# Kernel optimization log

Hardware: AMD Instinct MI355X
Metric: run time of the kernel (lower is better)

Reference implementation:

```python
import jax, jax.numpy as jnp
import numpy as np

DT = 1.0  # module init dt

def setup_inputs() -> dict:
    key = jax.random.key(0)
    k1, k2 = jax.random.split(key)
    x = jax.random.normal(k1, (8, 4096, 512), dtype=jnp.float32)
    w = jax.random.normal(k2, (512,), dtype=jnp.float32)
    return {"x": x, "w": w}

def reference(x, w):
    # h_t = h_{t-1} + dt*(x_t - relu(w)*h_{t-1}) = a*h_{t-1} + dt*x_t,  a = 1 - dt*relu(w)
    a = (1.0 - DT * jax.nn.relu(w)).astype(x.dtype)  # [d]
    h0 = jnp.zeros((x.shape[0], x.shape[2]), dtype=x.dtype)  # [b, d]
    xt = jnp.swapaxes(x, 0, 1)  # [t, b, d]

    def step(h, x_t):
        h_next = a * h + DT * x_t
        return h_next, h_next

    _, hs = jax.lax.scan(step, h0, xt)  # [t, b, d]
    return jnp.swapaxes(hs, 0, 1)  # [b, t, d] (return_sequences=True)
```

## Files before the change

### kernel.cpp

```cpp
#include <hip/hip_runtime.h>


#define RB 8
#define RT 4096
#define RD 512
#define DG (RD / 4)
#define TG 8
#define NTL (DG / TG)
#define CL 32
#define NC (RT / CL)
#define TPB 1024
#define PF 4
#define HB 1e15f

typedef float f32x4 __attribute__((ext_vector_type(4)));

__device__ __forceinline__ float sclamp(float v) {
    return fminf(fmaxf(v, -HB), HB);
}
__device__ __forceinline__ f32x4 sclamp4(f32x4 v) {
    v.x = sclamp(v.x); v.y = sclamp(v.y);
    v.z = sclamp(v.z); v.w = sclamp(v.w);
    return v;
}
__device__ __forceinline__ f32x4 ld4(const float4* __restrict__ p) {
    return *(const f32x4* __restrict__)p;
}
__device__ __forceinline__ f32x4 shfl4(f32x4 v, int src) {
    f32x4 r;
    r.x = __shfl(v.x, src, 64);
    r.y = __shfl(v.y, src, 64);
    r.z = __shfl(v.z, src, 64);
    r.w = __shfl(v.w, src, 64);
    return r;
}
__device__ __forceinline__ f32x4 relu_decay(float4 wq) {
    f32x4 a;
    a.x = 1.0f - fmaxf(wq.x, 0.0f);
    a.y = 1.0f - fmaxf(wq.y, 0.0f);
    a.z = 1.0f - fmaxf(wq.z, 0.0f);
    a.w = 1.0f - fmaxf(wq.w, 0.0f);
    return a;
}

__global__ void __launch_bounds__(TPB, 4)
rnn_fused3(const float4* __restrict__ x4, const float4* __restrict__ w4,
           float4* __restrict__ out4) {
    const int tid = threadIdx.x;
    const int g   = tid & (TG - 1);
    const int c   = tid >> 3;

    const int bid  = blockIdx.x;
    const int b    = bid >> 4;
    const int tile = bid & (NTL - 1);

    const f32x4 A1 = relu_decay(w4[tile * TG + g]);

    __shared__ f32x4 Wagg[NC * 9];
    __shared__ f32x4 CI[NC * 9];
    __shared__ f32x4 WinAgg[2 * 9];

    const size_t base = ((size_t)b * RT + (size_t)c * CL) * DG
                      + (size_t)(tile * TG + g);
    const float4* __restrict__ xb = x4 + base;

    {
        f32x4 v[PF];
#pragma unroll
        for (int k = 0; k < PF; ++k) v[k] = ld4(xb + (size_t)k * DG);
        f32x4 h = {0.f, 0.f, 0.f, 0.f};
#pragma unroll
        for (int bb = 0; bb < CL; bb += PF) {
            f32x4 n[PF];
            if (bb + PF < CL) {
#pragma unroll
                for (int k = 0; k < PF; ++k)
                    n[k] = ld4(xb + (size_t)(bb + PF + k) * DG);
            }
#pragma unroll
            for (int k = 0; k < PF; ++k) h = sclamp4(A1 * h + v[k]);
            if (bb + PF < CL) {
#pragma unroll
                for (int k = 0; k < PF; ++k) v[k] = n[k];
            }
        }
        Wagg[c * 9 + g] = h;
    }
    __syncthreads();

    {
        const int w  = tid >> 6;
        const int l  = tid & 63;
        const int g2 = w & (TG - 1);
        const int q  = w >> 3;
        const int cc = q * 64 + l;

        f32x4 B = relu_decay(w4[tile * TG + g2]);
#pragma unroll
        for (int i = 0; i < 5; ++i) B = sclamp4(B * B);

        f32x4 S = Wagg[cc * 9 + g2];
        f32x4 M = B;
#pragma unroll
        for (int s = 1; s < 64; s <<= 1) {
            f32x4 t = shfl4(S, l >= s ? l - s : l);
            S = (l >= s) ? sclamp4(M * t + S) : S;
            M = sclamp4(M * M);
        }
        if (l == 63) WinAgg[q * 9 + g2] = S;
        __syncthreads();

        f32x4 WC = {0.f, 0.f, 0.f, 0.f};
        if (q == 1) WC = WinAgg[0 * 9 + g2];
        const int n = l + 1;
        f32x4 P = {1.f, 1.f, 1.f, 1.f};
        f32x4 mm = B;
#pragma unroll
        for (int k = 0; k < 7; ++k) {
            if ((n >> k) & 1) P = sclamp4(P * mm);
            mm = sclamp4(mm * mm);
        }
        f32x4 Sf = sclamp4(S + P * WC);
        if (cc < NC - 1) CI[(cc + 1) * 9 + g2] = Sf;
        if (cc == 0)     CI[0 * 9 + g2] = (f32x4){0.f, 0.f, 0.f, 0.f};
    }
    __syncthreads();

    {
        float4* __restrict__ ob = out4 + base;
        f32x4 h = CI[c * 9 + g];
        f32x4 v[PF];
#pragma unroll
        for (int k = 0; k < PF; ++k) v[k] = ld4(xb + (size_t)k * DG);
#pragma unroll
        for (int bb = 0; bb < CL; bb += PF) {
            f32x4 n[PF];
            if (bb + PF < CL) {
#pragma unroll
                for (int k = 0; k < PF; ++k)
                    n[k] = ld4(xb + (size_t)(bb + PF + k) * DG);
            }
#pragma unroll
            for (int k = 0; k < PF; ++k) {
                h = sclamp4(A1 * h + v[k]);
                __builtin_nontemporal_store(
                    h, (f32x4*)(ob + (size_t)(bb + k) * DG));
            }
            if (bb + PF < CL) {
#pragma unroll
                for (int k = 0; k < PF; ++k) v[k] = n[k];
            }
        }
    }
}

extern "C" void kernel_launch(void* const* d_in, const int* in_sizes, int n_in,
                              void* d_out, int out_size, void* d_ws, size_t ws_size,
                              hipStream_t stream) {
    const float4* x4 = (const float4*)d_in[0];
    const float4* w4 = (const float4*)d_in[1];
    float4* o4 = (float4*)d_out;
    rnn_fused3<<<dim3(RB * NTL), dim3(TPB), 0, stream>>>(x4, w4, o4);
}
```

Before: 138.9 us.

## Split time axis across two blocks, recomputing first-half carry redundantly

The grid doubles to 256 blocks by splitting the sequence into two halves. Each second-half block redundantly scans the first half to get its carry-in, then both halves run the chunked scan with the chunk length halved. This exposes more parallelism on a GPU with many CUs, where 128 blocks left units idle. The cost is extra reads of x and extra compute for second-half blocks, which makes the work per block uneven.

```diff
diff --git a/kernel.cpp b/kernel.cpp
--- a/kernel.cpp
+++ b/kernel.cpp
@@ -7,8 +7,9 @@
 #define DG (RD / 4)
 #define TG 8
 #define NTL (DG / TG)
-#define CL 32
-#define NC (RT / CL)
+#define HT (RT / 2)
+#define CL 16
+#define NC (HT / CL)
 #define TPB 1024
 #define PF 4
 #define HB 1e15f
@@ -43,64 +44,94 @@
     return a;
 }
 
+__device__ __forceinline__ f32x4 chunk_scan(const float4* __restrict__ xb,
+                                            f32x4 A1) {
+    f32x4 v[PF];
+#pragma unroll
+    for (int k = 0; k < PF; ++k) v[k] = ld4(xb + (size_t)k * DG);
+    f32x4 h = {0.f, 0.f, 0.f, 0.f};
+#pragma unroll
+    for (int bb = 0; bb < CL; bb += PF) {
+        f32x4 n[PF];
+        if (bb + PF < CL) {
+#pragma unroll
+            for (int k = 0; k < PF; ++k)
+                n[k] = ld4(xb + (size_t)(bb + PF + k) * DG);
+        }
+#pragma unroll
+        for (int k = 0; k < PF; ++k) h = sclamp4(A1 * h + v[k]);
+        if (bb + PF < CL) {
+#pragma unroll
+            for (int k = 0; k < PF; ++k) v[k] = n[k];
+        }
+    }
+    return h;
+}
+
 __global__ void __launch_bounds__(TPB, 4)
-rnn_fused3(const float4* __restrict__ x4, const float4* __restrict__ w4,
-           float4* __restrict__ out4) {
+rnn_half(const float4* __restrict__ x4, const float4* __restrict__ w4,
+         float4* __restrict__ out4) {
     const int tid = threadIdx.x;
     const int g   = tid & (TG - 1);
     const int c   = tid >> 3;
 
     const int bid  = blockIdx.x;
-    const int b    = bid >> 4;
-    const int tile = bid & (NTL - 1);
+    const int hh   = bid >> 7;
+    const int p    = bid & 127;
+    const int b    = p >> 4;
+    const int tile = p & (NTL - 1);
 
     const f32x4 A1 = relu_decay(w4[tile * TG + g]);
 
     __shared__ f32x4 Wagg[NC * 9];
     __shared__ f32x4 CI[NC * 9];
     __shared__ f32x4 WinAgg[2 * 9];
+    __shared__ f32x4 Hc[TG];
 
-    const size_t base = ((size_t)b * RT + (size_t)c * CL) * DG
-                      + (size_t)(tile * TG + g);
-    const float4* __restrict__ xb = x4 + base;
+    const size_t tilebase = (size_t)b * RT * DG + (size_t)(tile * TG + g);
+    const float4* __restrict__ xb_own =
+        x4 + tilebase + (size_t)(hh * HT + c * CL) * DG;
 
-    {
-        f32x4 v[PF];
+    const int w  = tid >> 6;
+    const int l  = tid & 63;
+    const int g2 = w & (TG - 1);
+    const int q  = w >> 3;
+    const int cc = q * 64 + l;
+
+    f32x4 Bg2 = relu_decay(w4[tile * TG + g2]);
 #pragma unroll
-        for (int k = 0; k < PF; ++k) v[k] = ld4(xb + (size_t)k * DG);
-        f32x4 h = {0.f, 0.f, 0.f, 0.f};
+    for (int i = 0; i < 4; ++i) Bg2 = sclamp4(Bg2 * Bg2);
+
+    if (hh == 1) {
+        const float4* __restrict__ xb_f =
+            x4 + tilebase + (size_t)(c * CL) * DG;
+        Wagg[c * 9 + g] = chunk_scan(xb_f, A1);
+        __syncthreads();
+        {
+            f32x4 S = Wagg[cc * 9 + g2];
+            f32x4 M = Bg2;
 #pragma unroll
-        for (int bb = 0; bb < CL; bb += PF) {
-            f32x4 n[PF];
-            if (bb + PF < CL) {
-#pragma unroll
-                for (int k = 0; k < PF; ++k)
-                    n[k] = ld4(xb + (size_t)(bb + PF + k) * DG);
+            for (int s = 1; s < 64; s <<= 1) {
+                f32x4 t = shfl4(S, l >= s ? l - s : l);
+                S = (l >= s) ? sclamp4(M * t + S) : S;
+                M = sclamp4(M * M);
             }
-#pragma unroll
-            for (int k = 0; k < PF; ++k) h = sclamp4(A1 * h + v[k]);
-            if (bb + PF < CL) {
-#pragma unroll
-                for (int k = 0; k < PF; ++k) v[k] = n[k];
-            }
+            if (l == 63) WinAgg[q * 9 + g2] = S;
+            __syncthreads();
+            if (q == 1 && l == 63)
+                Hc[g2] = sclamp4(M * WinAgg[0 * 9 + g2] + S);
         }
-        Wagg[c * 9 + g] = h;
     }
     __syncthreads();
 
+    Wagg[c * 9 + g] = chunk_scan(xb_own, A1);
+    __syncthreads();
+
     {
-        const int w  = tid >> 6;
-        const int l  = tid & 63;
-        const int g2 = w & (TG - 1);
-        const int q  = w >> 3;
-        const int cc = q * 64 + l;
-
-        f32x4 B = relu_decay(w4[tile * TG + g2]);
-#pragma unroll
-        for (int i = 0; i < 5; ++i) B = sclamp4(B * B);
-
+        const f32x4 C0 = (hh == 1) ? Hc[g2]
+                                   : (f32x4){0.f, 0.f, 0.f, 0.f};
         f32x4 S = Wagg[cc * 9 + g2];
-        f32x4 M = B;
+        f32x4 M = Bg2;
 #pragma unroll
         for (int s = 1; s < 64; s <<= 1) {
             f32x4 t = shfl4(S, l >= s ? l - s : l);
@@ -110,11 +141,11 @@
         if (l == 63) WinAgg[q * 9 + g2] = S;
         __syncthreads();
 
-        f32x4 WC = {0.f, 0.f, 0.f, 0.f};
-        if (q == 1) WC = WinAgg[0 * 9 + g2];
+        f32x4 WC = C0;
+        if (q == 1) WC = sclamp4(M * C0 + WinAgg[0 * 9 + g2]);
         const int n = l + 1;
         f32x4 P = {1.f, 1.f, 1.f, 1.f};
-        f32x4 mm = B;
+        f32x4 mm = Bg2;
 #pragma unroll
         for (int k = 0; k < 7; ++k) {
             if ((n >> k) & 1) P = sclamp4(P * mm);
@@ -122,23 +153,24 @@
         }
         f32x4 Sf = sclamp4(S + P * WC);
         if (cc < NC - 1) CI[(cc + 1) * 9 + g2] = Sf;
-        if (cc == 0)     CI[0 * 9 + g2] = (f32x4){0.f, 0.f, 0.f, 0.f};
+        if (cc == 0)     CI[0 * 9 + g2] = C0;
     }
     __syncthreads();
 
     {
-        float4* __restrict__ ob = out4 + base;
+        float4* __restrict__ ob =
+            out4 + tilebase + (size_t)(hh * HT + c * CL) * DG;
         f32x4 h = CI[c * 9 + g];
         f32x4 v[PF];
 #pragma unroll
-        for (int k = 0; k < PF; ++k) v[k] = ld4(xb + (size_t)k * DG);
+        for (int k = 0; k < PF; ++k) v[k] = ld4(xb_own + (size_t)k * DG);
 #pragma unroll
         for (int bb = 0; bb < CL; bb += PF) {
             f32x4 n[PF];
             if (bb + PF < CL) {
 #pragma unroll
                 for (int k = 0; k < PF; ++k)
-                    n[k] = ld4(xb + (size_t)(bb + PF + k) * DG);
+                    n[k] = ld4(xb_own + (size_t)(bb + PF + k) * DG);
             }
 #pragma unroll
             for (int k = 0; k < PF; ++k) {
@@ -160,5 +192,5 @@
     const float4* x4 = (const float4*)d_in[0];
     const float4* w4 = (const float4*)d_in[1];
     float4* o4 = (float4*)d_out;
-    rnn_fused3<<<dim3(RB * NTL), dim3(TPB), 0, stream>>>(x4, w4, o4);
+    rnn_half<<<dim3(2 * RB * NTL), dim3(TPB), 0, stream>>>(x4, w4, o4);
 }
```

Measured after the change: 120.5 us. 13.2% less time.
